# Optimization experiments

Measured on AMD Instinct MI355X. Metric: run time of the kernel, lower is better.

## Reference

```python
import jax, jax.numpy as jnp
import numpy as np

B, S, H, I = 2, 2048, 4096, 16384
EPS = 1e-12


def setup_inputs() -> dict:
    key = jax.random.key(0)
    ks = jax.random.split(key, 8)
    w_scale = 0.02
    return {
        "input": jax.random.normal(ks[0], (B, S, H), jnp.float32),
        "residual": jax.random.normal(ks[1], (B, S, H), jnp.float32),
        "bias": jax.random.normal(ks[2], (H,), jnp.float32) * w_scale,
        "attn_nw": jnp.ones((H,), jnp.float32),
        "attn_nb": jnp.zeros((H,), jnp.float32),
        "inter_w": jax.random.normal(ks[3], (I, H), jnp.float32) * w_scale,
        "inter_b": jax.random.normal(ks[4], (I,), jnp.float32) * w_scale,
        "output_w": jax.random.normal(ks[5], (H, I), jnp.float32) * w_scale,
        "output_b": jax.random.normal(ks[6], (H,), jnp.float32) * w_scale,
    }


def reference(input, residual, bias, attn_nw, attn_nb, inter_w, inter_b, output_w, output_b):
    # Fused mlp_gemm: residual_add = input + residual + attn-output bias
    residual_add = input + residual + bias  # [B,S,H]
    # LayerNorm over hidden dim with attn_nw/attn_nb
    mean = jnp.mean(residual_add, axis=-1, keepdims=True)
    var = jnp.var(residual_add, axis=-1, keepdims=True)
    ln = (residual_add - mean) * jax.lax.rsqrt(var + EPS) * attn_nw + attn_nb
    # Intermediate GEMM + bias + GELU (DeepSpeed uses tanh-approx gelu)
    inter = jax.nn.gelu(jnp.einsum("bsh,ih->bsi", ln, inter_w) + inter_b, approximate=True)
    # Output projection (vector_matmul)
    out = jnp.einsum("bsi,hi->bsh", inter, output_w)
    # bias_residual: add residual_add and output bias
    return out + residual_add + output_b
```

## Files before the change

### kernel.cpp

```cpp
#include <hip/hip_runtime.h>
#include <hip/hip_bf16.h>
#include <cstdint>
#include <math.h>

typedef __attribute__((ext_vector_type(4))) float f32x4;
typedef __attribute__((ext_vector_type(8))) __bf16 bf16x8;

__device__ __forceinline__ unsigned short f2bf(float f) {
    union { float f; unsigned u; } v; v.f = f;
    unsigned u = v.u + 0x7fffu + ((v.u >> 16) & 1u);
    return (unsigned short)(u >> 16);
}

__device__ __forceinline__ float gelu_tanh(float x) {
    float x3 = x * x * x;
    float t = tanhf(0.7978845608028654f * (x + 0.044715f * x3));
    return 0.5f * x * (1.0f + t);
}

__device__ __forceinline__ void gload_lds16(const void* g, void* l) {
    __builtin_amdgcn_global_load_lds(
        (__attribute__((address_space(1))) void*)(uintptr_t)g,
        (__attribute__((address_space(3))) void*)(unsigned)(uintptr_t)l,
        16, 0, 0);
}

__global__ __launch_bounds__(256)
void fused_add_ln(const float* __restrict__ in, const float* __restrict__ res,
                  const float* __restrict__ bias, const float* __restrict__ nw,
                  const float* __restrict__ nb, float* __restrict__ resadd,
                  unsigned short* __restrict__ lnout, int H) {
    const int row = blockIdx.x;
    const int tid = threadIdx.x;
    const size_t base = (size_t)row * H;
    float v[16];
    float s = 0.f, ss = 0.f;
#pragma unroll
    for (int i = 0; i < 4; ++i) {
        int idx = (i * 256 + tid) * 4;
        float4 a = *(const float4*)(in + base + idx);
        float4 b = *(const float4*)(res + base + idx);
        float4 c = *(const float4*)(bias + idx);
        float x0 = a.x + b.x + c.x, x1 = a.y + b.y + c.y;
        float x2 = a.z + b.z + c.z, x3 = a.w + b.w + c.w;
        v[i * 4 + 0] = x0; v[i * 4 + 1] = x1; v[i * 4 + 2] = x2; v[i * 4 + 3] = x3;
        s += x0 + x1 + x2 + x3;
        ss += x0 * x0 + x1 * x1 + x2 * x2 + x3 * x3;
    }
#pragma unroll
    for (int off = 32; off > 0; off >>= 1) {
        s += __shfl_down(s, off);
        ss += __shfl_down(ss, off);
    }
    __shared__ float red[8];
    const int w = tid >> 6;
    if ((tid & 63) == 0) { red[w] = s; red[4 + w] = ss; }
    __syncthreads();
    s = red[0] + red[1] + red[2] + red[3];
    ss = red[4] + red[5] + red[6] + red[7];
    const float mean = s / H;
    const float var = ss / H - mean * mean;
    const float rstd = rsqrtf(var + 1e-12f);
#pragma unroll
    for (int i = 0; i < 4; ++i) {
        int idx = (i * 256 + tid) * 4;
        float4 wv = *(const float4*)(nw + idx);
        float4 bv = *(const float4*)(nb + idx);
        float4 r;
        r.x = v[i * 4 + 0]; r.y = v[i * 4 + 1]; r.z = v[i * 4 + 2]; r.w = v[i * 4 + 3];
        *(float4*)(resadd + base + idx) = r;
        ushort4 o;
        o.x = f2bf((r.x - mean) * rstd * wv.x + bv.x);
        o.y = f2bf((r.y - mean) * rstd * wv.y + bv.y);
        o.z = f2bf((r.z - mean) * rstd * wv.z + bv.z);
        o.w = f2bf((r.w - mean) * rstd * wv.w + bv.w);
        *(ushort4*)(lnout + base + idx) = o;
    }
}

__global__ __launch_bounds__(256)
void cast_w(const float* __restrict__ w, unsigned short* __restrict__ o, long long n4) {
    long long i = (long long)blockIdx.x * 256 + threadIdx.x;
    if (i >= n4) return;
    float4 f = *(const float4*)(w + i * 4);
    ushort4 u;
    u.x = f2bf(f.x); u.y = f2bf(f.y); u.z = f2bf(f.z); u.w = f2bf(f.w);
    *(ushort4*)(o + i * 4) = u;
}

#define GBM 256
#define GBN 256

#define STAGE(s, mat, h, T) do {                                              \
    const unsigned short* _src = ((mat) ? pB : pA)                            \
        + (size_t)((h) * 128) * K + (size_t)(T) * 64;                         \
    char* _dst = ldsc + (s) * 65536 + (mat) * 32768 + (h) * 16384 + dOff;     \
    gload_lds16(_src, _dst);                                                  \
    gload_lds16(_src + (size_t)64 * K, _dst + 8192);                          \
} while (0)

#define STG(s, T) do { STAGE(s, 0, 0, T); STAGE(s, 0, 1, T);                  \
                       STAGE(s, 1, 0, T); STAGE(s, 1, 1, T); } while (0)

#define RD_B(s) do {                                                          \
    _Pragma("unroll")                                                         \
    for (int ni = 0; ni < 4; ++ni)                                            \
        _Pragma("unroll")                                                     \
        for (int kk = 0; kk < 2; ++kk)                                        \
            bq[ni][kk] = *(const bf16x8*)(ldsc + (s) * 65536 + 32768          \
                + ((wc * 64 + ni * 16 + lrow) << 7) + ckk[kk]);               \
} while (0)

#define RD_A(bk, q, s) do {                                                   \
    _Pragma("unroll")                                                         \
    for (int m2 = 0; m2 < 2; ++m2)                                            \
        _Pragma("unroll")                                                     \
        for (int kk = 0; kk < 2; ++kk)                                        \
            aq[bk][m2][kk] = *(const bf16x8*)(ldsc + (s) * 65536              \
                + ((wr * 128 + ((q) * 2 + m2) * 16 + lrow) << 7) + ckk[kk]);  \
} while (0)

#define MF(q, bk) do {                                                        \
    __builtin_amdgcn_s_setprio(1);                                            \
    _Pragma("unroll")                                                         \
    for (int m2 = 0; m2 < 2; ++m2)                                            \
        _Pragma("unroll")                                                     \
        for (int ni = 0; ni < 4; ++ni)                                        \
            _Pragma("unroll")                                                 \
            for (int kk = 0; kk < 2; ++kk)                                    \
                acc[(q) * 2 + m2][ni] = __builtin_amdgcn_mfma_f32_16x16x32_bf16( \
                    aq[bk][m2][kk], bq[ni][kk], acc[(q) * 2 + m2][ni], 0, 0, 0); \
    __builtin_amdgcn_s_setprio(0);                                            \
} while (0)

#define WAITP do { asm volatile("s_waitcnt lgkmcnt(0)" ::: "memory");         \
                   __builtin_amdgcn_sched_barrier(0); } while (0)
#define SB0   __builtin_amdgcn_sched_barrier(0)
#define BAR   asm volatile("s_barrier" ::: "memory")
#define GATE0 asm volatile("s_waitcnt vmcnt(0)" ::: "memory")

template <int EPI>
__global__ __launch_bounds__(512, 2)
void gemm256(const unsigned short* __restrict__ A,
             const unsigned short* __restrict__ B,
             const float* __restrict__ bias_n,
             const float* __restrict__ resadd,
             void* __restrict__ Cout,
             int M, int N, int K) {
    __shared__ unsigned short lds[2][2][2][128 * 64];
    char* ldsc = (char*)&lds[0][0][0][0];
    const int tid = threadIdx.x;
    const int lane = tid & 63;
    const int w = tid >> 6;
    const int wr = w >> 2;
    const int wc = w & 3;

    const int nwg = gridDim.x;
    const int lg = (blockIdx.x & 7) * (nwg >> 3) + (blockIdx.x >> 3);
    const int nbx = N / GBN;
    const int brow = lg / nbx;
    const int bcol = lg % nbx;

    const int srow = tid >> 3;
    const int scol = ((((tid & 7) << 4) ^ ((srow & 7) << 4)) >> 1);
    const unsigned short* pA = A + (size_t)(brow * GBM + srow) * K + scol;
    const unsigned short* pB = B + (size_t)(bcol * GBN + srow) * K + scol;
    const int dOff = tid * 16;

    const int lrow = lane & 15;
    int ckk[2];
    ckk[0] = (((lane >> 4) << 4)) ^ ((lrow & 7) << 4);
    ckk[1] = ckk[0] ^ 64;

    f32x4 acc[8][4] = {};
    bf16x8 aq[2][2][2];
    bf16x8 bq[4][2];

    const int NT = K / 64;
    const int niter = NT / 2;

    STG(0, 0);
    GATE0; BAR;
    RD_B(0); RD_A(0, 0, 0);

    for (int i = 0; i < niter - 1; ++i) {
        const int T1 = 2 * i + 1, T2 = 2 * i + 2;
        WAITP; RD_A(1, 1, 0); STG(1, T1); SB0; MF(0, 0);
        WAITP; RD_A(0, 2, 0);             SB0; MF(1, 1);
        WAITP; RD_A(1, 3, 0);             SB0; MF(2, 0);
        WAITP; GATE0; BAR; RD_A(0, 0, 1); SB0; MF(3, 1); RD_B(1);
        WAITP; RD_A(1, 1, 1); STG(0, T2); SB0; MF(0, 0);
        WAITP; RD_A(0, 2, 1);             SB0; MF(1, 1);
        WAITP; RD_A(1, 3, 1);             SB0; MF(2, 0);
        WAITP; GATE0; BAR; RD_A(0, 0, 0); SB0; MF(3, 1); RD_B(0);
    }
    {
        WAITP; RD_A(1, 1, 0); STG(1, NT - 1); SB0; MF(0, 0);
        WAITP; RD_A(0, 2, 0);                 SB0; MF(1, 1);
        WAITP; RD_A(1, 3, 0);                 SB0; MF(2, 0);
        WAITP; GATE0; BAR; RD_A(0, 0, 1);     SB0; MF(3, 1); RD_B(1);
        WAITP; RD_A(1, 1, 1);                 SB0; MF(0, 0);
        WAITP; RD_A(0, 2, 1);                 SB0; MF(1, 1);
        WAITP; RD_A(1, 3, 1);                 SB0; MF(2, 0);
        WAITP;                                     MF(3, 1);
    }

    const int c0 = bcol * GBN + wc * 64 + lrow;
    const int r0 = brow * GBM + wr * 128 + (lane >> 4) * 4;
#pragma unroll
    for (int mi = 0; mi < 8; ++mi) {
#pragma unroll
        for (int j = 0; j < 4; ++j) {
            const int row = r0 + mi * 16 + j;
#pragma unroll
            for (int ni = 0; ni < 4; ++ni) {
                const int col = c0 + ni * 16;
                float x = acc[mi][ni][j] + bias_n[col];
                if (EPI == 0) {
                    ((unsigned short*)Cout)[(size_t)row * N + col] = f2bf(gelu_tanh(x));
                } else {
                    const size_t off = (size_t)row * N + col;
                    ((float*)Cout)[off] = x + resadd[off];
                }
            }
        }
    }
}

extern "C" void kernel_launch(void* const* d_in, const int* in_sizes, int n_in,
                              void* d_out, int out_size, void* d_ws, size_t ws_size,
                              hipStream_t stream) {
    const float* input    = (const float*)d_in[0];
    const float* residual = (const float*)d_in[1];
    const float* bias     = (const float*)d_in[2];
    const float* attn_nw  = (const float*)d_in[3];
    const float* attn_nb  = (const float*)d_in[4];
    const float* inter_w  = (const float*)d_in[5];
    const float* inter_b  = (const float*)d_in[6];
    const float* output_w = (const float*)d_in[7];
    const float* output_b = (const float*)d_in[8];

    const int H = in_sizes[3];
    const int I = in_sizes[6];
    const int T = in_sizes[0] / H;

    char* ws = (char*)d_ws;
    float* resadd      = (float*)ws;
    unsigned short* ln = (unsigned short*)(ws + (size_t)T * H * 4);
    unsigned short* w1 = (unsigned short*)((char*)ln + (size_t)T * H * 2);
    unsigned short* w2 = w1 + (size_t)I * H;
    unsigned short* act = w2 + (size_t)H * I;

    fused_add_ln<<<T, 256, 0, stream>>>(input, residual, bias, attn_nw, attn_nb,
                                        resadd, ln, H);

    {
        long long n4 = (long long)I * H / 4;
        int blocks = (int)((n4 + 255) / 256);
        cast_w<<<blocks, 256, 0, stream>>>(inter_w, w1, n4);
        cast_w<<<blocks, 256, 0, stream>>>(output_w, w2, n4);
    }

    {
        dim3 grid((T / GBM) * (I / GBN));
        gemm256<0><<<grid, 512, 0, stream>>>(ln, w1, inter_b, nullptr, act, T, I, H);
    }

    {
        dim3 grid((T / GBM) * (H / GBN));
        gemm256<1><<<grid, 512, 0, stream>>>(act, w2, output_b, resadd, d_out, T, H, I);
    }
}
```

Before: 1.211 ms.

## Reschedule GEMM main loop with partial lgkmcnt waits and split staging

```diff
diff --git a/kernel.cpp b/kernel.cpp
--- a/kernel.cpp
+++ b/kernel.cpp
@@ -99,9 +99,6 @@
     gload_lds16(_src + (size_t)64 * K, _dst + 8192);                          \
 } while (0)
 
-#define STG(s, T) do { STAGE(s, 0, 0, T); STAGE(s, 0, 1, T);                  \
-                       STAGE(s, 1, 0, T); STAGE(s, 1, 1, T); } while (0)
-
 #define RD_B(s) do {                                                          \
     _Pragma("unroll")                                                         \
     for (int ni = 0; ni < 4; ++ni)                                            \
@@ -123,18 +120,20 @@
 #define MF(q, bk) do {                                                        \
     __builtin_amdgcn_s_setprio(1);                                            \
     _Pragma("unroll")                                                         \
-    for (int m2 = 0; m2 < 2; ++m2)                                            \
+    for (int kk = 0; kk < 2; ++kk)                                            \
         _Pragma("unroll")                                                     \
-        for (int ni = 0; ni < 4; ++ni)                                        \
+        for (int m2 = 0; m2 < 2; ++m2)                                        \
             _Pragma("unroll")                                                 \
-            for (int kk = 0; kk < 2; ++kk)                                    \
+            for (int ni = 0; ni < 4; ++ni)                                    \
                 acc[(q) * 2 + m2][ni] = __builtin_amdgcn_mfma_f32_16x16x32_bf16( \
                     aq[bk][m2][kk], bq[ni][kk], acc[(q) * 2 + m2][ni], 0, 0, 0); \
     __builtin_amdgcn_s_setprio(0);                                            \
 } while (0)
 
-#define WAITP do { asm volatile("s_waitcnt lgkmcnt(0)" ::: "memory");         \
-                   __builtin_amdgcn_sched_barrier(0); } while (0)
+#define LG4 do { asm volatile("s_waitcnt lgkmcnt(4)" ::: "memory");           \
+                 __builtin_amdgcn_sched_barrier(0); } while (0)
+#define LG0 do { asm volatile("s_waitcnt lgkmcnt(0)" ::: "memory");           \
+                 __builtin_amdgcn_sched_barrier(0); } while (0)
 #define SB0   __builtin_amdgcn_sched_barrier(0)
 #define BAR   asm volatile("s_barrier" ::: "memory")
 #define GATE0 asm volatile("s_waitcnt vmcnt(0)" ::: "memory")
@@ -179,30 +178,48 @@
     const int NT = K / 64;
     const int niter = NT / 2;
 
-    STG(0, 0);
+    STAGE(0, 1, 0, 0); STAGE(0, 1, 1, 0);
+    STAGE(0, 0, 0, 0); STAGE(0, 0, 1, 0);
     GATE0; BAR;
-    RD_B(0); RD_A(0, 0, 0);
+    RD_A(0, 0, 0);
 
     for (int i = 0; i < niter - 1; ++i) {
         const int T1 = 2 * i + 1, T2 = 2 * i + 2;
-        WAITP; RD_A(1, 1, 0); STG(1, T1); SB0; MF(0, 0);
-        WAITP; RD_A(0, 2, 0);             SB0; MF(1, 1);
-        WAITP; RD_A(1, 3, 0);             SB0; MF(2, 0);
-        WAITP; GATE0; BAR; RD_A(0, 0, 1); SB0; MF(3, 1); RD_B(1);
-        WAITP; RD_A(1, 1, 1); STG(0, T2); SB0; MF(0, 0);
-        WAITP; RD_A(0, 2, 1);             SB0; MF(1, 1);
-        WAITP; RD_A(1, 3, 1);             SB0; MF(2, 0);
-        WAITP; GATE0; BAR; RD_A(0, 0, 0); SB0; MF(3, 1); RD_B(0);
-    }
-    {
-        WAITP; RD_A(1, 1, 0); STG(1, NT - 1); SB0; MF(0, 0);
-        WAITP; RD_A(0, 2, 0);                 SB0; MF(1, 1);
-        WAITP; RD_A(1, 3, 0);                 SB0; MF(2, 0);
-        WAITP; GATE0; BAR; RD_A(0, 0, 1);     SB0; MF(3, 1); RD_B(1);
-        WAITP; RD_A(1, 1, 1);                 SB0; MF(0, 0);
-        WAITP; RD_A(0, 2, 1);                 SB0; MF(1, 1);
-        WAITP; RD_A(1, 3, 1);                 SB0; MF(2, 0);
-        WAITP;                                     MF(3, 1);
+        RD_B(0); SB0; RD_A(1, 1, 0); BAR;
+        STAGE(1, 0, 0, T1); STAGE(1, 0, 1, T1); LG4; MF(0, 0);
+        RD_A(0, 2, 0); BAR;
+        STAGE(1, 1, 0, T1); STAGE(1, 1, 1, T1); LG4; MF(1, 1);
+        RD_A(1, 3, 0); GATE0; BAR;
+        LG4; MF(2, 0);
+        RD_A(0, 0, 1); BAR;
+        LG4; MF(3, 1);
+        RD_B(1); SB0; RD_A(1, 1, 1); BAR;
+        STAGE(0, 0, 0, T2); STAGE(0, 0, 1, T2); LG4; MF(0, 0);
+        RD_A(0, 2, 1); BAR;
+        STAGE(0, 1, 0, T2); STAGE(0, 1, 1, T2); LG4; MF(1, 1);
+        RD_A(1, 3, 1); GATE0; BAR;
+        LG4; MF(2, 0);
+        RD_A(0, 0, 0); BAR;
+        LG4; MF(3, 1);
+    }
+    {
+        const int T1 = NT - 1;
+        RD_B(0); SB0; RD_A(1, 1, 0); BAR;
+        STAGE(1, 0, 0, T1); STAGE(1, 0, 1, T1); LG4; MF(0, 0);
+        RD_A(0, 2, 0); BAR;
+        STAGE(1, 1, 0, T1); STAGE(1, 1, 1, T1); LG4; MF(1, 1);
+        RD_A(1, 3, 0); GATE0; BAR;
+        LG4; MF(2, 0);
+        RD_A(0, 0, 1); BAR;
+        LG4; MF(3, 1);
+        RD_B(1); SB0; RD_A(1, 1, 1); BAR;
+        LG4; MF(0, 0);
+        RD_A(0, 2, 1); BAR;
+        LG4; MF(1, 1);
+        RD_A(1, 3, 1); BAR;
+        LG4; MF(2, 0);
+        BAR;
+        LG0; MF(3, 1);
     }
 
     const int c0 = bcol * GBN + wc * 64 + lrow;
```

Measured after the change: 1.298 ms. 7.1% more time.
